# Kernel optimization log

Hardware: AMD Instinct MI355X
Metric: run time of the kernel (lower is better)

Reference implementation:

```python
import jax, jax.numpy as jnp
import numpy as np

B, N, DIM, HEADS = 4, 1024, 1024, 16
DH = DIM // HEADS
SCALE = 1.0 / np.sqrt(DH)
EPS = 1e-6


def clinear(x, Wr, Wi, br, bi):
    # (a+bi)(Wr+Wi i): real = a Wr^T - b Wi^T, imag = a Wi^T + b Wr^T
    xr, xi = x.real, x.imag
    real = xr @ Wr.T - xi @ Wi.T + br
    imag = xr @ Wi.T + xi @ Wr.T + bi
    return jax.lax.complex(real, imag)


def cln(x, gamma, beta):
    # normalize magnitude over last dim, keep phase
    mag = jnp.abs(x)
    phase = jnp.angle(x)
    mean = jnp.mean(mag, axis=-1, keepdims=True)
    var = jnp.var(mag, axis=-1, keepdims=True)
    nm = (mag - mean) / jnp.sqrt(var + EPS)
    nm = nm * gamma + beta
    return jax.lax.complex(nm * jnp.cos(phase), nm * jnp.sin(phase))


def forward(xr, xi, Wq_r, Wq_i, bq_r, bq_i, Wk_r, Wk_i, bk_r, bk_i,
            Wv_r, Wv_i, bv_r, bv_i, Wo_r, Wo_i, bo_r, bo_i,
            gq, beq, gk, bek, gv, bev):
    x = jax.lax.complex(xr, xi)  # [B,N,D] complex64

    def heads(t):
        return t.reshape(B, N, HEADS, DH).transpose(0, 2, 1, 3)  # [B,H,N,dh]

    Q = heads(cln(clinear(x, Wq_r, Wq_i, bq_r, bq_i), gq, beq))
    K = heads(cln(clinear(x, Wk_r, Wk_i, bk_r, bk_i), gk, bek))
    V = heads(cln(clinear(x, Wv_r, Wv_i, bv_r, bv_i), gv, bev))

    Qf = jnp.fft.fft(Q, axis=2, norm='ortho')
    Kf = jnp.fft.fft(K, axis=2, norm='ortho')
    Vf = jnp.fft.fft(V, axis=2, norm='ortho')

    scores = jnp.einsum('bhnd,bhmd->bhnm', Qf, jnp.conj(Kf)) * SCALE
    attn = jax.nn.softmax(scores.real, axis=-1)  # real-valued softmax
    # attn is real; multiply into complex Vf componentwise
    out_f = jax.lax.complex(jnp.einsum('bhnm,bhmd->bhnd', attn, Vf.real),
                            jnp.einsum('bhnm,bhmd->bhnd', attn, Vf.imag))
    out = jnp.fft.ifft(out_f, axis=2, norm='ortho')
    out = out.transpose(0, 2, 1, 3).reshape(B, N, DIM)
    y = clinear(out, Wo_r, Wo_i, bo_r, bo_i)
    # return real||imag concatenated on last axis (float32 view of complex output)
    return jnp.concatenate([y.real, y.imag], axis=-1)


def setup_inputs() -> dict:
    key = jax.random.key(0)
    ks = jax.random.split(key, 16)
    wscale = np.sqrt(2.0 / (DIM + DIM)).astype(np.float32)
    d = {}
    d['xr'] = jax.random.normal(ks[0], (B, N, DIM), jnp.float32)
    d['xi'] = jax.random.normal(ks[1], (B, N, DIM), jnp.float32)
    i = 2
    for name in ('q', 'k', 'v', 'o'):
        d[f'W{name}_r'] = jax.random.normal(ks[i], (DIM, DIM), jnp.float32) * wscale; i += 1
        d[f'W{name}_i'] = jax.random.normal(ks[i], (DIM, DIM), jnp.float32) * wscale; i += 1
        d[f'b{name}_r'] = jnp.zeros((DIM,), jnp.float32)
        d[f'b{name}_i'] = jnp.zeros((DIM,), jnp.float32)
    for name in ('q', 'k', 'v'):
        d[f'g{name}'] = jnp.ones((DIM,), jnp.float32)
        d[f'be{name}'] = jnp.zeros((DIM,), jnp.float32)
    return d


def reference(xr, xi, Wq_r, Wq_i, bq_r, bq_i, Wk_r, Wk_i, bk_r, bk_i,
              Wv_r, Wv_i, bv_r, bv_i, Wo_r, Wo_i, bo_r, bo_i,
              gq, beq, gk, bek, gv, bev):
    return forward(xr, xi, Wq_r, Wq_i, bq_r, bq_i, Wk_r, Wk_i, bk_r, bk_i,
                   Wv_r, Wv_i, bv_r, bv_i, Wo_r, Wo_i, bo_r, bo_i,
                   gq, beq, gk, bek, gv, bev)
```

## Files before the change

### kernel.cpp

```cpp
#include <hip/hip_runtime.h>
#include <math.h>

#define BB 4
#define NN 1024
#define DIMM 1024
#define HHH 16
#define DHH 64
#define BN 4096
#define EPS_LN 1e-6f

typedef __bf16 bf16_t;
typedef __bf16 bf16x8 __attribute__((ext_vector_type(8)));
typedef __bf16 bf16x4 __attribute__((ext_vector_type(4)));
typedef float f32x4 __attribute__((ext_vector_type(4)));
typedef float f32x16 __attribute__((ext_vector_type(16)));
#define MFMA16(a, b, c) __builtin_amdgcn_mfma_f32_16x16x32_bf16(a, b, c, 0, 0, 0)
#define MFMA32(a, b, c) __builtin_amdgcn_mfma_f32_32x32x16_bf16(a, b, c, 0, 0, 0)
#define AS1 __attribute__((address_space(1)))
#define AS3 __attribute__((address_space(3)))

__device__ inline unsigned pk2(float a, float b) {
  union { bf16_t h[2]; unsigned u; } c;
  c.h[0] = (bf16_t)a; c.h[1] = (bf16_t)b;
  return c.u;
}
union U16 { uint4 u; bf16x8 v; };

__global__ __launch_bounds__(256) void pack_x(
    const float* __restrict__ xr, const float* __restrict__ xi,
    bf16_t* __restrict__ out)
{
  int t = blockIdx.x * 256 + threadIdx.x;
  size_t e = (size_t)t * 8;
  int row = (int)(e >> 11), col = (int)(e & 2047);
  const float* src = (col < 1024) ? (xr + (size_t)row * 1024 + col)
                                  : (xi + (size_t)row * 1024 + col - 1024);
  float4 a = *(const float4*)src;
  float4 b = *(const float4*)(src + 4);
  bf16x8 o;
  o[0] = (bf16_t)a.x; o[1] = (bf16_t)a.y; o[2] = (bf16_t)a.z; o[3] = (bf16_t)a.w;
  o[4] = (bf16_t)b.x; o[5] = (bf16_t)b.y; o[6] = (bf16_t)b.z; o[7] = (bf16_t)b.w;
  *(bf16x8*)(out + e) = o;
}

__global__ __launch_bounds__(256) void pack_w4(
    const float* __restrict__ Wqr, const float* __restrict__ Wqi,
    const float* __restrict__ bqr, const float* __restrict__ bqi,
    const float* __restrict__ Wkr, const float* __restrict__ Wki,
    const float* __restrict__ bkr, const float* __restrict__ bki,
    const float* __restrict__ Wvr, const float* __restrict__ Wvi,
    const float* __restrict__ bvr, const float* __restrict__ bvi,
    const float* __restrict__ Wor, const float* __restrict__ Woi,
    const float* __restrict__ bor, const float* __restrict__ boi,
    bf16_t* __restrict__ Wcat4, float* __restrict__ bcat4)
{
  const int p = blockIdx.y;
  const float* Wr; const float* Wi; const float* br; const float* bi;
  if (p == 0)      { Wr = Wqr; Wi = Wqi; br = bqr; bi = bqi; }
  else if (p == 1) { Wr = Wkr; Wi = Wki; br = bkr; bi = bki; }
  else if (p == 2) { Wr = Wvr; Wi = Wvi; br = bvr; bi = bvi; }
  else             { Wr = Wor; Wi = Woi; br = bor; bi = boi; }
  bf16_t* Wcat = Wcat4 + (size_t)p * 2048 * 2048;
  float*  bcat = bcat4 + (size_t)p * 2048;

  int t = blockIdx.x * 256 + threadIdx.x;
  size_t e = (size_t)t * 8;
  int row = (int)(e >> 11), col = (int)(e & 2047);
  const float* src;
  float sgn = 1.f;
  if (row < 1024) {
    if (col < 1024) src = Wr + (size_t)row * 1024 + col;
    else          { src = Wi + (size_t)row * 1024 + col - 1024; sgn = -1.f; }
  } else {
    int r2 = row - 1024;
    if (col < 1024) src = Wi + (size_t)r2 * 1024 + col;
    else            src = Wr + (size_t)r2 * 1024 + col - 1024;
  }
  float4 a = *(const float4*)src;
  float4 b = *(const float4*)(src + 4);
  bf16x8 o;
  o[0] = (bf16_t)(sgn * a.x); o[1] = (bf16_t)(sgn * a.y);
  o[2] = (bf16_t)(sgn * a.z); o[3] = (bf16_t)(sgn * a.w);
  o[4] = (bf16_t)(sgn * b.x); o[5] = (bf16_t)(sgn * b.y);
  o[6] = (bf16_t)(sgn * b.z); o[7] = (bf16_t)(sgn * b.w);
  *(bf16x8*)(Wcat + e) = o;
  if (e < 2048) {
#pragma unroll
    for (int j = 0; j < 8; ++j) {
      int n = (int)e + j;
      bcat[n] = (n < 1024) ? br[n] : bi[n - 1024];
    }
  }
}

__global__ __launch_bounds__(256) void gemm_qkv(
    const bf16_t* __restrict__ A, const bf16_t* __restrict__ Bt,
    const float* __restrict__ bias, bf16_t* __restrict__ C6)
{
  __shared__ bf16_t sA[128 * 64];
  __shared__ bf16_t sB[128 * 64];
  const int tid = threadIdx.x;
  const int w = tid >> 6, l = tid & 63;
  const int lo4 = l & 15, hi = l >> 4;
  const int wr = w >> 1, wc = w & 1;
  const int row0 = blockIdx.y * 128, col0 = blockIdx.x * 128;

  const int srow = (l >> 3);
  const int scol = (l & 7) * 8;
  const bf16_t* gA[4];
  const bf16_t* gB[4];
#pragma unroll
  for (int i = 0; i < 4; ++i) {
    int r = (w * 4 + i) * 8 + srow;
    gA[i] = A  + (size_t)(row0 + r) * 2048 + scol;
    gB[i] = Bt + (size_t)(col0 + r) * 2048 + scol;
  }

  f32x4 acc[4][4] = {};
  for (int k0 = 0; k0 < 2048; k0 += 64) {
    __syncthreads();
#pragma unroll
    for (int i = 0; i < 4; ++i) {
      __builtin_amdgcn_global_load_lds((const AS1 void*)(gA[i] + k0),
                                       (AS3 void*)&sA[(w * 4 + i) * 512], 16, 0, 0);
      __builtin_amdgcn_global_load_lds((const AS1 void*)(gB[i] + k0),
                                       (AS3 void*)&sB[(w * 4 + i) * 512], 16, 0, 0);
    }
    __syncthreads();
#pragma unroll
    for (int kk = 0; kk < 2; ++kk) {
      bf16x8 am[4], bn[4];
#pragma unroll
      for (int i = 0; i < 4; ++i)
        am[i] = *(const bf16x8*)&sA[(wr * 64 + i * 16 + lo4) * 64 + kk * 32 + hi * 8];
#pragma unroll
      for (int j = 0; j < 4; ++j)
        bn[j] = *(const bf16x8*)&sB[(wc * 64 + j * 16 + lo4) * 64 + kk * 32 + hi * 8];
#pragma unroll
      for (int i = 0; i < 4; ++i)
#pragma unroll
        for (int j = 0; j < 4; ++j)
          acc[i][j] = MFMA16(am[i], bn[j], acc[i][j]);
    }
  }
  const int colg0 = col0 + wc * 64;
#pragma unroll
  for (int i = 0; i < 4; ++i) {
#pragma unroll
    for (int j = 0; j < 4; ++j) {
      float bv = bias[colg0 + j * 16 + lo4];
#pragma unroll
      for (int r = 0; r < 4; ++r) {
        int rowg = row0 + wr * 64 + i * 16 + hi * 4 + r;
        C6[(size_t)rowg * 6144 + colg0 + j * 16 + lo4] = (bf16_t)(acc[i][j][r] + bv);
      }
    }
  }
}

__global__ __launch_bounds__(256) void gemm_bf16(
    const bf16_t* __restrict__ A, const bf16_t* __restrict__ Bt,
    const float* __restrict__ bias,
    float* __restrict__ Cr, float* __restrict__ Ci, int ldc)
{
  __shared__ bf16_t sA[128 * 64];
  __shared__ bf16_t sB[128 * 64];
  const int tid = threadIdx.x;
  const int w = tid >> 6, l = tid & 63;
  const int lo4 = l & 15, hi = l >> 4;
  const int wr = w >> 1, wc = w & 1;
  const int row0 = blockIdx.y * 128, col0 = blockIdx.x * 128;

  const int srow = (l >> 3);
  const int scol = (l & 7) * 8;
  const bf16_t* gA[4];
  const bf16_t* gB[4];
#pragma unroll
  for (int i = 0; i < 4; ++i) {
    int r = (w * 4 + i) * 8 + srow;
    gA[i] = A  + (size_t)(row0 + r) * 2048 + scol;
    gB[i] = Bt + (size_t)(col0 + r) * 2048 + scol;
  }

  f32x4 acc[4][4] = {};
  for (int k0 = 0; k0 < 2048; k0 += 64) {
    __syncthreads();
#pragma unroll
    for (int i = 0; i < 4; ++i) {
      __builtin_amdgcn_global_load_lds((const AS1 void*)(gA[i] + k0),
                                       (AS3 void*)&sA[(w * 4 + i) * 512], 16, 0, 0);
      __builtin_amdgcn_global_load_lds((const AS1 void*)(gB[i] + k0),
                                       (AS3 void*)&sB[(w * 4 + i) * 512], 16, 0, 0);
    }
    __syncthreads();
#pragma unroll
    for (int kk = 0; kk < 2; ++kk) {
      bf16x8 am[4], bn[4];
#pragma unroll
      for (int i = 0; i < 4; ++i)
        am[i] = *(const bf16x8*)&sA[(wr * 64 + i * 16 + lo4) * 64 + kk * 32 + hi * 8];
#pragma unroll
      for (int j = 0; j < 4; ++j)
        bn[j] = *(const bf16x8*)&sB[(wc * 64 + j * 16 + lo4) * 64 + kk * 32 + hi * 8];
#pragma unroll
      for (int i = 0; i < 4; ++i)
#pragma unroll
        for (int j = 0; j < 4; ++j)
          acc[i][j] = MFMA16(am[i], bn[j], acc[i][j]);
    }
  }
  const int colg0 = col0 + wc * 64;
  float* Cp = (colg0 < 1024) ? Cr : Ci;
  const int cb = colg0 & 1023;
#pragma unroll
  for (int i = 0; i < 4; ++i) {
#pragma unroll
    for (int j = 0; j < 4; ++j) {
      float bv = bias[colg0 + j * 16 + lo4];
#pragma unroll
      for (int r = 0; r < 4; ++r) {
        int rowg = row0 + wr * 64 + i * 16 + hi * 4 + r;
        Cp[(size_t)rowg * ldc + cb + j * 16 + lo4] = acc[i][j][r] + bv;
      }
    }
  }
}

__global__ __launch_bounds__(256) void ln_stats3(
    const bf16_t* __restrict__ C6, float2* __restrict__ st)
{
  __shared__ float red[8];
  const int row = blockIdx.x;
  const int p = blockIdx.y;
  const int tid = threadIdx.x;
  const bf16_t* pr = C6 + (size_t)row * 6144 + p * 2048;
  const bf16_t* pi = pr + 1024;
  bf16x4 vr = *(const bf16x4*)(pr + tid * 4);
  bf16x4 vi = *(const bf16x4*)(pi + tid * 4);
  float s = 0.f, s2 = 0.f;
#pragma unroll
  for (int t = 0; t < 4; ++t) {
    float a = (float)vr[t], b = (float)vi[t];
    float mg = sqrtf(a * a + b * b);
    s += mg; s2 += mg * mg;
  }
#pragma unroll
  for (int o = 32; o; o >>= 1) { s += __shfl_down(s, o); s2 += __shfl_down(s2, o); }
  if ((tid & 63) == 0) { red[tid >> 6] = s; red[4 + (tid >> 6)] = s2; }
  __syncthreads();
  if (tid == 0) {
    float S = red[0] + red[1] + red[2] + red[3];
    float S2 = red[4] + red[5] + red[6] + red[7];
    float mean = S * (1.f / DIMM);
    float var = S2 * (1.f / DIMM) - mean * mean;
    st[(size_t)p * 4096 + row] = make_float2(mean, rsqrtf(var + EPS_LN));
  }
}

#define LIDX(d_, c_) (((d_) << 10) + ((c_) ^ (((c_) >> 5) & 31) ^ (((d_) & 7) << 2)))

__global__ __launch_bounds__(512) void fft_kernel(
    const bf16_t* __restrict__ inR, const bf16_t* __restrict__ inI,
    bf16_t* __restrict__ outR, bf16_t* __restrict__ outI,
    int in_sb, int in_sh, int in_sn, int in_sd,
    int out_sb, int out_sh, int out_sn,
    float sign, float oscale, int imode, int omode,
    const float2* __restrict__ stats,
    const float* __restrict__ gamma, const float* __restrict__ beta)
{
  __shared__ float lr[8 * 1024], li[8 * 1024];
  __shared__ float2 tw[1024];
  const int tid = threadIdx.x;
  const int dc = blockIdx.x & 7;
  const int bh = blockIdx.x >> 3;
  const int b = bh >> 4, h = bh & 15;
  const bf16_t* bR = inR + (size_t)b * in_sb + (size_t)h * in_sh;
  const bf16_t* bI = inI + (size_t)b * in_sb + (size_t)h * in_sh;
#pragma unroll
  for (int t = tid; t < 1024; t += 512) {
    float ang = sign * 3.14159265358979323846f * (float)t * (1.f / 512.f);
    float sn, cs;
    __sincosf(ang, &sn, &cs);
    tw[t] = make_float2(cs, sn);
  }
  if (imode == 0) {
    float gg[8], bb[8];
    if (stats) {
#pragma unroll
      for (int ds = 0; ds < 8; ++ds) {
        gg[ds] = gamma[h * DHH + dc * 8 + ds];
        bb[ds] = beta[h * DHH + dc * 8 + ds];
      }
    }
#pragma unroll
    for (int rep = 0; rep < 2; ++rep) {
      int n = tid + rep * 512;
      bf16x8 r8 = *(const bf16x8*)(bR + (size_t)n * in_sn + dc * 8);
      bf16x8 i8 = *(const bf16x8*)(bI + (size_t)n * in_sn + dc * 8);
      float ur[8], ui[8];
#pragma unroll
      for (int ds = 0; ds < 8; ++ds) { ur[ds] = (float)r8[ds]; ui[ds] = (float)i8[ds]; }
      if (stats) {
        float2 stv = stats[b * NN + n];
#pragma unroll
        for (int ds = 0; ds < 8; ++ds) {
          float a = ur[ds], c2 = ui[ds];
          float mag = sqrtf(a * a + c2 * c2);
          float nm = (mag - stv.x) * stv.y * gg[ds] + bb[ds];
          if (mag > 0.f) { float sc = nm / mag; ur[ds] = a * sc; ui[ds] = c2 * sc; }
          else           { ur[ds] = nm; ui[ds] = 0.f; }
        }
      }
#pragma unroll
      for (int ds = 0; ds < 8; ++ds) {
        int ax = LIDX(ds, n);
        lr[ax] = ur[ds];
        li[ax] = ui[ds];
      }
    }
  } else {
    const int ds = tid & 7, nb = tid >> 3;
    const bf16_t* pR = bR + (size_t)(dc * 8 + ds) * in_sd + nb * 16;
    const bf16_t* pI = bI + (size_t)(dc * 8 + ds) * in_sd + nb * 16;
    bf16x8 a0 = *(const bf16x8*)pR, a1 = *(const bf16x8*)(pR + 8);
    bf16x8 b0 = *(const bf16x8*)pI, b1 = *(const bf16x8*)(pI + 8);
#pragma unroll
    for (int k = 0; k < 8; ++k) {
      int c = nb * 16 + k;
      lr[LIDX(ds, c)] = (float)a0[k];       li[LIDX(ds, c)] = (float)b0[k];
      lr[LIDX(ds, c + 8)] = (float)a1[k];   li[LIDX(ds, c + 8)] = (float)b1[k];
    }
  }
  __syncthreads();
  const int dsub = tid & 7;
  const int jb = tid >> 3;
  int lq2 = 8;
  for (int st = 0; st < 5; ++st) {
    const int qtr = 1 << lq2;
    const int tmul = 1 << (2 * st);
    for (int jt = 0; jt < 4; ++jt) {
      int j = jb + jt * 64;
      int o = j & (qtr - 1);
      int i0 = ((j >> lq2) << (lq2 + 2)) + o;
      int a0 = LIDX(dsub, i0);
      int a1 = LIDX(dsub, i0 + qtr);
      int a2 = LIDX(dsub, i0 + 2 * qtr);
      int a3 = LIDX(dsub, i0 + 3 * qtr);
      float x0r = lr[a0], x0i = li[a0];
      float x1r = lr[a1], x1i = li[a1];
      float x2r = lr[a2], x2i = li[a2];
      float x3r = lr[a3], x3i = li[a3];
      float ar = x0r + x2r, ai2 = x0i + x2i;
      float br = x0r - x2r, bi  = x0i - x2i;
      float cr = x1r + x3r, ci  = x1i + x3i;
      float dr = x1r - x3r, di  = x1i - x3i;
      float2 t1 = tw[o * tmul];
      float2 t2 = tw[2 * o * tmul];
      float2 t3 = tw[3 * o * tmul];
      lr[a0] = ar + cr;  li[a0] = ai2 + ci;
      float u1r = br - sign * di, u1i = bi + sign * dr;
      lr[a1] = u1r * t1.x - u1i * t1.y;  li[a1] = u1r * t1.y + u1i * t1.x;
      float u2r = ar - cr, u2i = ai2 - ci;
      lr[a2] = u2r * t2.x - u2i * t2.y;  li[a2] = u2r * t2.y + u2i * t2.x;
      float u3r = br + sign * di, u3i = bi - sign * dr;
      lr[a3] = u3r * t3.x - u3i * t3.y;  li[a3] = u3r * t3.y + u3i * t3.x;
    }
    __syncthreads();
    lq2 -= 2;
  }
  bf16_t* oRb = outR + (size_t)b * out_sb + (size_t)h * out_sh;
  bf16_t* oIb = outI + (size_t)b * out_sb + (size_t)h * out_sh;
#pragma unroll
  for (int rep = 0; rep < 2; ++rep) {
    int n = tid + rep * 512;
    int rv2 = __brev((unsigned)n) >> 22;
    int p = ((rv2 & 0x155) << 1) | ((rv2 >> 1) & 0x155);
    float fr[8], fi[8];
#pragma unroll
    for (int ds = 0; ds < 8; ++ds) {
      fr[ds] = lr[LIDX(ds, p)] * oscale;
      fi[ds] = li[LIDX(ds, p)] * oscale;
    }
    if (omode == 1) {
      size_t tb = (size_t)(n >> 5) * 4096;
#pragma unroll
      for (int ds = 0; ds < 8; ++ds) {
        int dch = dc * 8 + ds;
        size_t ga = tb + (size_t)dch * 32 + ((n & 31) ^ (((dch >> 1) & 3) << 3));
        oRb[ga] = (bf16_t)fr[ds];
        oIb[ga] = (bf16_t)fi[ds];
      }
    } else {
      int cb = dc * 8;
      if (omode == 2) cb = (dc ^ (n & 7)) * 8;
      bf16x8 v0, w0;
#pragma unroll
      for (int k = 0; k < 8; ++k) {
        v0[k] = (bf16_t)fr[k];
        w0[k] = (bf16_t)fi[k];
      }
      size_t gb = (size_t)n * out_sn + cb;
      *(bf16x8*)(oRb + gb) = v0;
      *(bf16x8*)(oIb + gb) = w0;
    }
  }
}

__global__ __launch_bounds__(256, 2) void fattn(
    const bf16_t* __restrict__ Qf, const bf16_t* __restrict__ Kfs,
    const bf16_t* __restrict__ Vfs, bf16_t* __restrict__ OT)
{
  __shared__ bf16_t K3[3][4096];
  __shared__ bf16_t V3[3][4096];
  const int tid = threadIdx.x;
  const int w = tid >> 6, l = tid & 63;
  const int lq = l & 31;
  const int h = l >> 5;
  const int i = blockIdx.x;
  const int j = i >> 3;
  const int bh = (i & 7) * 8 + (j >> 3);
  const int q0 = (j & 7) * 128 + w * 32;

  bf16x8 bq[8];
  const bf16_t* qp = Qf + ((size_t)bh * NN + q0 + lq) * 128 + h * 8;
#pragma unroll
  for (int kk = 0; kk < 8; ++kk) bq[kk] = *(const bf16x8*)(qp + kk * 16);

  f32x16 o[4] = {};
  float m = -3e38f, ln = 0.f;

  const bf16_t* kg = Kfs + (size_t)bh * 131072 + w * 1024 + l * 8;
  const bf16_t* vg = Vfs + (size_t)bh * 131072 + w * 1024 + l * 8;
  const int kswz = (lq & 7) << 3;
  const int vswz = ((lq >> 1) & 3) << 3;

#pragma unroll
  for (int tt = 0; tt < 2; ++tt) {
    const bf16_t* kt = kg + (size_t)tt * 4096;
    const bf16_t* vt = vg + (size_t)tt * 4096;
#pragma unroll
    for (int ii = 0; ii < 2; ++ii) {
      __builtin_amdgcn_global_load_lds((const AS1 void*)(kt + ii * 512),
                                       (AS3 void*)&K3[tt][w * 1024 + ii * 512], 16, 0, 0);
      __builtin_amdgcn_global_load_lds((const AS1 void*)(vt + ii * 512),
                                       (AS3 void*)&V3[tt][w * 1024 + ii * 512], 16, 0, 0);
    }
  }
  asm volatile("s_waitcnt vmcnt(4)" ::: "memory");
  __builtin_amdgcn_s_barrier();
  __builtin_amdgcn_sched_barrier(0);

  int cur = 0;
  for (int t = 0; t < 32; ++t) {
    if (t < 30) {
      int nb = cur + 2; if (nb >= 3) nb -= 3;
      const bf16_t* kt = kg + (size_t)(t + 2) * 4096;
      const bf16_t* vt = vg + (size_t)(t + 2) * 4096;
#pragma unroll
      for (int ii = 0; ii < 2; ++ii) {
        __builtin_amdgcn_global_load_lds((const AS1 void*)(kt + ii * 512),
                                         (AS3 void*)&K3[nb][w * 1024 + ii * 512], 16, 0, 0);
        __builtin_amdgcn_global_load_lds((const AS1 void*)(vt + ii * 512),
                                         (AS3 void*)&V3[nb][w * 1024 + ii * 512], 16, 0, 0);
      }
    }

    f32x16 s = {};
#pragma unroll
    for (int kk = 0; kk < 8; ++kk) {
      bf16x8 ak = *(const bf16x8*)&K3[cur][lq * 128 + ((kk * 16 + h * 8) ^ kswz)];
      s = MFMA32(ak, bq[kk], s);
    }

    float pmax = s[0];
#pragma unroll
    for (int r = 1; r < 16; ++r) pmax = fmaxf(pmax, s[r]);
    pmax = fmaxf(pmax, __shfl_xor(pmax, 32));
    if (!__all(pmax - m <= 8.f)) {
      float mnew = fmaxf(m, pmax);
      float alpha = __expf(m - mnew);
      m = mnew;
      ln *= alpha;
#pragma unroll
      for (int db = 0; db < 4; ++db)
#pragma unroll
        for (int r = 0; r < 16; ++r) o[db][r] *= alpha;
    }
    float pf[16];
    float rs = 0.f;
#pragma unroll
    for (int r = 0; r < 16; ++r) { pf[r] = __expf(s[r] - m); rs += pf[r]; }
    rs += __shfl_xor(rs, 32);
    ln += rs;

    unsigned pw[8];
#pragma unroll
    for (int ii = 0; ii < 8; ++ii) pw[ii] = pk2(pf[2 * ii], pf[2 * ii + 1]);
    unsigned r0 = (unsigned)__shfl_xor((int)(h ? pw[0] : pw[2]), 32);
    unsigned r1 = (unsigned)__shfl_xor((int)(h ? pw[1] : pw[3]), 32);
    unsigned r2 = (unsigned)__shfl_xor((int)(h ? pw[4] : pw[6]), 32);
    unsigned r3 = (unsigned)__shfl_xor((int)(h ? pw[5] : pw[7]), 32);
    U16 bp0, bp1;
    bp0.u.x = h ? r0 : pw[0];  bp0.u.y = h ? r1 : pw[1];
    bp0.u.z = h ? pw[2] : r0;  bp0.u.w = h ? pw[3] : r1;
    bp1.u.x = h ? r2 : pw[4];  bp1.u.y = h ? r3 : pw[5];
    bp1.u.z = h ? pw[6] : r2;  bp1.u.w = h ? pw[7] : r3;

#pragma unroll
    for (int db = 0; db < 4; ++db) {
      int r = db * 32 + lq;
      bf16x8 av0 = *(const bf16x8*)&V3[cur][r * 32 + ((h * 8) ^ vswz)];
      bf16x8 av1 = *(const bf16x8*)&V3[cur][r * 32 + ((16 + h * 8) ^ vswz)];
      o[db] = MFMA32(av0, bp0.v, o[db]);
      o[db] = MFMA32(av1, bp1.v, o[db]);
    }

    if (t < 31) {
      if (t < 30) asm volatile("s_waitcnt vmcnt(4)" ::: "memory");
      else        asm volatile("s_waitcnt vmcnt(0)" ::: "memory");
      __builtin_amdgcn_s_barrier();
      __builtin_amdgcn_sched_barrier(0);
    }
    cur = (cur == 2) ? 0 : cur + 1;
  }

  float inv = 1.f / ln;
  const size_t otb = (size_t)bh * 128 * NN + q0 + lq;
#pragma unroll
  for (int db = 0; db < 4; ++db)
#pragma unroll
    for (int r = 0; r < 16; ++r) {
      int dl = (r & 3) + 8 * (r >> 2) + 4 * h;
      OT[otb + (size_t)(db * 32 + dl) * NN] = (bf16_t)(o[db][r] * inv);
    }
}

extern "C" void kernel_launch(void* const* d_in, const int* in_sizes, int n_in,
                              void* d_out, int out_size, void* d_ws, size_t ws_size,
                              hipStream_t stream) {
  const float* xr   = (const float*)d_in[0];
  const float* xi   = (const float*)d_in[1];
  const float* Wqr  = (const float*)d_in[2];
  const float* Wqi  = (const float*)d_in[3];
  const float* bqr  = (const float*)d_in[4];
  const float* bqi  = (const float*)d_in[5];
  const float* Wkr  = (const float*)d_in[6];
  const float* Wki  = (const float*)d_in[7];
  const float* bkr  = (const float*)d_in[8];
  const float* bki  = (const float*)d_in[9];
  const float* Wvr  = (const float*)d_in[10];
  const float* Wvi  = (const float*)d_in[11];
  const float* bvr  = (const float*)d_in[12];
  const float* bvi  = (const float*)d_in[13];
  const float* Wor  = (const float*)d_in[14];
  const float* Woi  = (const float*)d_in[15];
  const float* bor  = (const float*)d_in[16];
  const float* boi  = (const float*)d_in[17];
  const float* gq   = (const float*)d_in[18];
  const float* beq  = (const float*)d_in[19];
  const float* gk   = (const float*)d_in[20];
  const float* bek  = (const float*)d_in[21];
  const float* gv   = (const float*)d_in[22];
  const float* bev  = (const float*)d_in[23];

  char* wp = (char*)d_ws;
  bf16_t* Axaug = (bf16_t*)wp;  wp += (size_t)4096 * 2048 * 2;
  bf16_t* Wcat4 = (bf16_t*)wp;  wp += (size_t)8192 * 2048 * 2;
  float*  bcat4 = (float*)wp;   wp += (size_t)8192 * 4;
  float2* lnst3 = (float2*)wp;  wp += (size_t)3 * 4096 * 8;
  bf16_t* C6    = (bf16_t*)wp;  wp += (size_t)4096 * 6144 * 2;
  bf16_t* Qf    = (bf16_t*)wp;  wp += (size_t)64 * 1024 * 128 * 2;
  bf16_t* Kf    = (bf16_t*)wp;  wp += (size_t)64 * 1024 * 128 * 2;
  bf16_t* VfT   = (bf16_t*)wp;  wp += (size_t)64 * 1024 * 128 * 2;
  bf16_t* OT    = C6;
  bf16_t* Yaug  = Qf;

  const dim3 gQKV(48, 32);
  const dim3 gGemmO(16, 32);
  const int gPackX = (4096 * 2048 / 8) / 256;
  const dim3 gPackW(2048, 4);
  const dim3 gLn(4096, 3);
  const int gFft = 64 * 8;
  const int gAtt = 64 * 8;

  pack_x<<<gPackX, 256, 0, stream>>>(xr, xi, Axaug);
  pack_w4<<<gPackW, 256, 0, stream>>>(Wqr, Wqi, bqr, bqi,
                                      Wkr, Wki, bkr, bki,
                                      Wvr, Wvi, bvr, bvi,
                                      Wor, Woi, bor, boi,
                                      Wcat4, bcat4);

  gemm_qkv<<<gQKV, 256, 0, stream>>>(Axaug, Wcat4, bcat4, C6);
  ln_stats3<<<gLn, 256, 0, stream>>>(C6, lnst3);

  fft_kernel<<<gFft, 512, 0, stream>>>(C6, C6 + 1024, Qf, Qf + 64,
      NN * 6144, DHH, 6144, 1,
      16 * NN * 128, NN * 128, 128,
      -1.0f, 0.03125f * 0.125f, 0, 0, lnst3, gq, beq);
  fft_kernel<<<gFft, 512, 0, stream>>>(C6 + 2048, C6 + 3072, Kf, Kf + 64,
      NN * 6144, DHH, 6144, 1,
      16 * NN * 128, NN * 128, 128,
      -1.0f, 0.03125f, 0, 2, lnst3 + 4096, gk, bek);
  fft_kernel<<<gFft, 512, 0, stream>>>(C6 + 4096, C6 + 5120, VfT, VfT + 2048,
      NN * 6144, DHH, 6144, 1,
      16 * 131072, 131072, 0,
      -1.0f, 0.03125f, 0, 1, lnst3 + 8192, gv, bev);

  fattn<<<gAtt, 256, 0, stream>>>(Qf, Kf, VfT, OT);

  fft_kernel<<<gFft, 512, 0, stream>>>(OT, OT + (size_t)64 * NN, Yaug, Yaug + 1024,
      16 * 128 * NN, 128 * NN, 1, NN,
      NN * 2048, 64, 2048,
      +1.0f, 0.03125f, 1, 0, nullptr, nullptr, nullptr);

  float* yout = (float*)d_out;
  gemm_bf16<<<gGemmO, 256, 0, stream>>>(Yaug,
      Wcat4 + (size_t)3 * 2048 * 2048, bcat4 + 3 * 2048,
      yout, yout + 1024, 2048);
}
```

Measured before the change: 404.3 us.

## Remap GEMM tiles per XCD for L2 reuse and merge Q/K/V FFT launches

```diff
diff --git a/kernel.cpp b/kernel.cpp
--- a/kernel.cpp
+++ b/kernel.cpp
@@ -103,7 +103,12 @@
   const int w = tid >> 6, l = tid & 63;
   const int lo4 = l & 15, hi = l >> 4;
   const int wr = w >> 1, wc = w & 1;
-  const int row0 = blockIdx.y * 128, col0 = blockIdx.x * 128;
+  const int fid = blockIdx.y * 48 + blockIdx.x;
+  const int xcd = fid & 7;
+  const int rr2 = fid >> 3;
+  const int bx = xcd * 6 + (rr2 >> 5);
+  const int by = rr2 & 31;
+  const int row0 = by * 128, col0 = bx * 128;
 
   const int srow = (l >> 3);
   const int scol = (l & 7) * 8;
@@ -169,7 +174,12 @@
   const int w = tid >> 6, l = tid & 63;
   const int lo4 = l & 15, hi = l >> 4;
   const int wr = w >> 1, wc = w & 1;
-  const int row0 = blockIdx.y * 128, col0 = blockIdx.x * 128;
+  const int fid = blockIdx.y * 16 + blockIdx.x;
+  const int xcd = fid & 7;
+  const int rr2 = fid >> 3;
+  const int bx = xcd * 2 + (rr2 >> 5);
+  const int by = rr2 & 31;
+  const int row0 = by * 128, col0 = bx * 128;
 
   const int srow = (l >> 3);
   const int scol = (l & 7) * 8;
@@ -259,14 +269,149 @@
 
 #define LIDX(d_, c_) (((d_) << 10) + ((c_) ^ (((c_) >> 5) & 31) ^ (((d_) & 7) << 2)))
 
+__global__ __launch_bounds__(512) void fft_qkv(
+    const bf16_t* __restrict__ C6,
+    bf16_t* __restrict__ Qf, bf16_t* __restrict__ Kf, bf16_t* __restrict__ VfT,
+    const float2* __restrict__ lnst3,
+    const float* __restrict__ gq, const float* __restrict__ beq,
+    const float* __restrict__ gk, const float* __restrict__ bek,
+    const float* __restrict__ gv, const float* __restrict__ bev)
+{
+  __shared__ float lr[8 * 1024], li[8 * 1024];
+  __shared__ float2 tw[1024];
+  const int tid = threadIdx.x;
+  const int dc = blockIdx.x & 7;
+  const int bh = blockIdx.x >> 3;
+  const int b = bh >> 4, h = bh & 15;
+  const int which = blockIdx.y;
+
+  const bf16_t* inR = C6 + which * 2048;
+  const bf16_t* inI = inR + 1024;
+  const float2* stats = lnst3 + which * 4096;
+  const float* gamma = (which == 0) ? gq : (which == 1) ? gk : gv;
+  const float* beta  = (which == 0) ? beq : (which == 1) ? bek : bev;
+  const float oscale = (which == 0) ? (0.03125f * 0.125f) : 0.03125f;
+  const int omode = (which == 0) ? 0 : (which == 1) ? 2 : 1;
+  bf16_t* outR = (which == 0) ? Qf : (which == 1) ? Kf : VfT;
+  bf16_t* outI = outR + ((which == 2) ? 2048 : 64);
+
+  const bf16_t* bR = inR + (size_t)b * (NN * 6144) + (size_t)h * DHH;
+  const bf16_t* bI = inI + (size_t)b * (NN * 6144) + (size_t)h * DHH;
+#pragma unroll
+  for (int t = tid; t < 1024; t += 512) {
+    float ang = -3.14159265358979323846f * (float)t * (1.f / 512.f);
+    float sn, cs;
+    __sincosf(ang, &sn, &cs);
+    tw[t] = make_float2(cs, sn);
+  }
+  {
+    float gg[8], bb[8];
+#pragma unroll
+    for (int ds = 0; ds < 8; ++ds) {
+      gg[ds] = gamma[h * DHH + dc * 8 + ds];
+      bb[ds] = beta[h * DHH + dc * 8 + ds];
+    }
+#pragma unroll
+    for (int rep = 0; rep < 2; ++rep) {
+      int n = tid + rep * 512;
+      bf16x8 r8 = *(const bf16x8*)(bR + (size_t)n * 6144 + dc * 8);
+      bf16x8 i8 = *(const bf16x8*)(bI + (size_t)n * 6144 + dc * 8);
+      float2 stv = stats[b * NN + n];
+#pragma unroll
+      for (int ds = 0; ds < 8; ++ds) {
+        float a = (float)r8[ds], c2 = (float)i8[ds];
+        float mag = sqrtf(a * a + c2 * c2);
+        float nm = (mag - stv.x) * stv.y * gg[ds] + bb[ds];
+        float re, im;
+        if (mag > 0.f) { float sc = nm / mag; re = a * sc; im = c2 * sc; }
+        else           { re = nm; im = 0.f; }
+        int ax = LIDX(ds, n);
+        lr[ax] = re;
+        li[ax] = im;
+      }
+    }
+  }
+  __syncthreads();
+  const int dsub = tid & 7;
+  const int jb = tid >> 3;
+  int lq2 = 8;
+  for (int st = 0; st < 5; ++st) {
+    const int qtr = 1 << lq2;
+    const int tmul = 1 << (2 * st);
+    for (int jt = 0; jt < 4; ++jt) {
+      int j = jb + jt * 64;
+      int o = j & (qtr - 1);
+      int i0 = ((j >> lq2) << (lq2 + 2)) + o;
+      int a0 = LIDX(dsub, i0);
+      int a1 = LIDX(dsub, i0 + qtr);
+      int a2 = LIDX(dsub, i0 + 2 * qtr);
+      int a3 = LIDX(dsub, i0 + 3 * qtr);
+      float x0r = lr[a0], x0i = li[a0];
+      float x1r = lr[a1], x1i = li[a1];
+      float x2r = lr[a2], x2i = li[a2];
+      float x3r = lr[a3], x3i = li[a3];
+      float ar = x0r + x2r, ai2 = x0i + x2i;
+      float br = x0r - x2r, bi  = x0i - x2i;
+      float cr = x1r + x3r, ci  = x1i + x3i;
+      float dr = x1r - x3r, di  = x1i - x3i;
+      float2 t1 = tw[o * tmul];
+      float2 t2 = tw[2 * o * tmul];
+      float2 t3 = tw[3 * o * tmul];
+      lr[a0] = ar + cr;  li[a0] = ai2 + ci;
+      float u1r = br + di, u1i = bi - dr;
+      lr[a1] = u1r * t1.x - u1i * t1.y;  li[a1] = u1r * t1.y + u1i * t1.x;
+      float u2r = ar - cr, u2i = ai2 - ci;
+      lr[a2] = u2r * t2.x - u2i * t2.y;  li[a2] = u2r * t2.y + u2i * t2.x;
+      float u3r = br - di, u3i = bi + dr;
+      lr[a3] = u3r * t3.x - u3i * t3.y;  li[a3] = u3r * t3.y + u3i * t3.x;
+    }
+    __syncthreads();
+    lq2 -= 2;
+  }
+  bf16_t* oRb = outR + (size_t)b * 2097152 + (size_t)h * 131072;
+  bf16_t* oIb = outI + (size_t)b * 2097152 + (size_t)h * 131072;
+#pragma unroll
+  for (int rep = 0; rep < 2; ++rep) {
+    int n = tid + rep * 512;
+    int rv2 = __brev((unsigned)n) >> 22;
+    int p = ((rv2 & 0x155) << 1) | ((rv2 >> 1) & 0x155);
+    float fr[8], fi[8];
+#pragma unroll
+    for (int ds = 0; ds < 8; ++ds) {
+      fr[ds] = lr[LIDX(ds, p)] * oscale;
+      fi[ds] = li[LIDX(ds, p)] * oscale;
+    }
+    if (omode == 1) {
+      size_t tb = (size_t)(n >> 5) * 4096;
+#pragma unroll
+      for (int ds = 0; ds < 8; ++ds) {
+        int dch = dc * 8 + ds;
+        size_t ga = tb + (size_t)dch * 32 + ((n & 31) ^ (((dch >> 1) & 3) << 3));
+        oRb[ga] = (bf16_t)fr[ds];
+        oIb[ga] = (bf16_t)fi[ds];
+      }
+    } else {
+      int cb = dc * 8;
+      if (omode == 2) cb = (dc ^ (n & 7)) * 8;
+      bf16x8 v0, w0;
+#pragma unroll
+      for (int k = 0; k < 8; ++k) {
+        v0[k] = (bf16_t)fr[k];
+        w0[k] = (bf16_t)fi[k];
+      }
+      size_t gb = (size_t)n * 128 + cb;
+      *(bf16x8*)(oRb + gb) = v0;
+      *(bf16x8*)(oIb + gb) = w0;
+    }
+  }
+}
+
 __global__ __launch_bounds__(512) void fft_kernel(
     const bf16_t* __restrict__ inR, const bf16_t* __restrict__ inI,
     bf16_t* __restrict__ outR, bf16_t* __restrict__ outI,
     int in_sb, int in_sh, int in_sn, int in_sd,
     int out_sb, int out_sh, int out_sn,
-    float sign, float oscale, int imode, int omode,
-    const float2* __restrict__ stats,
-    const float* __restrict__ gamma, const float* __restrict__ beta)
+    float sign, float oscale)
 {
   __shared__ float lr[8 * 1024], li[8 * 1024];
   __shared__ float2 tw[1024];
@@ -283,42 +428,7 @@
     __sincosf(ang, &sn, &cs);
     tw[t] = make_float2(cs, sn);
   }
-  if (imode == 0) {
-    float gg[8], bb[8];
-    if (stats) {
-#pragma unroll
-      for (int ds = 0; ds < 8; ++ds) {
-        gg[ds] = gamma[h * DHH + dc * 8 + ds];
-        bb[ds] = beta[h * DHH + dc * 8 + ds];
-      }
-    }
-#pragma unroll
-    for (int rep = 0; rep < 2; ++rep) {
-      int n = tid + rep * 512;
-      bf16x8 r8 = *(const bf16x8*)(bR + (size_t)n * in_sn + dc * 8);
-      bf16x8 i8 = *(const bf16x8*)(bI + (size_t)n * in_sn + dc * 8);
-      float ur[8], ui[8];
-#pragma unroll
-      for (int ds = 0; ds < 8; ++ds) { ur[ds] = (float)r8[ds]; ui[ds] = (float)i8[ds]; }
-      if (stats) {
-        float2 stv = stats[b * NN + n];
-#pragma unroll
-        for (int ds = 0; ds < 8; ++ds) {
-          float a = ur[ds], c2 = ui[ds];
-          float mag = sqrtf(a * a + c2 * c2);
-          float nm = (mag - stv.x) * stv.y * gg[ds] + bb[ds];
-          if (mag > 0.f) { float sc = nm / mag; ur[ds] = a * sc; ui[ds] = c2 * sc; }
-          else           { ur[ds] = nm; ui[ds] = 0.f; }
-        }
-      }
-#pragma unroll
-      for (int ds = 0; ds < 8; ++ds) {
-        int ax = LIDX(ds, n);
-        lr[ax] = ur[ds];
-        li[ax] = ui[ds];
-      }
-    }
-  } else {
+  {
     const int ds = tid & 7, nb = tid >> 3;
     const bf16_t* pR = bR + (size_t)(dc * 8 + ds) * in_sd + nb * 16;
     const bf16_t* pI = bI + (size_t)(dc * 8 + ds) * in_sd + nb * 16;
@@ -381,28 +491,16 @@
       fr[ds] = lr[LIDX(ds, p)] * oscale;
       fi[ds] = li[LIDX(ds, p)] * oscale;
     }
-    if (omode == 1) {
-      size_t tb = (size_t)(n >> 5) * 4096;
-#pragma unroll
-      for (int ds = 0; ds < 8; ++ds) {
-        int dch = dc * 8 + ds;
-        size_t ga = tb + (size_t)dch * 32 + ((n & 31) ^ (((dch >> 1) & 3) << 3));
-        oRb[ga] = (bf16_t)fr[ds];
-        oIb[ga] = (bf16_t)fi[ds];
-      }
-    } else {
-      int cb = dc * 8;
-      if (omode == 2) cb = (dc ^ (n & 7)) * 8;
-      bf16x8 v0, w0;
-#pragma unroll
-      for (int k = 0; k < 8; ++k) {
-        v0[k] = (bf16_t)fr[k];
-        w0[k] = (bf16_t)fi[k];
-      }
-      size_t gb = (size_t)n * out_sn + cb;
-      *(bf16x8*)(oRb + gb) = v0;
-      *(bf16x8*)(oIb + gb) = w0;
-    }
+    int cb = dc * 8;
+    bf16x8 v0, w0;
+#pragma unroll
+    for (int k = 0; k < 8; ++k) {
+      v0[k] = (bf16_t)fr[k];
+      w0[k] = (bf16_t)fi[k];
+    }
+    size_t gb = (size_t)n * out_sn + cb;
+    *(bf16x8*)(oRb + gb) = v0;
+    *(bf16x8*)(oIb + gb) = w0;
   }
 }
 
@@ -580,6 +678,7 @@
   const int gPackX = (4096 * 2048 / 8) / 256;
   const dim3 gPackW(2048, 4);
   const dim3 gLn(4096, 3);
+  const dim3 gFftQKV(512, 3);
   const int gFft = 64 * 8;
   const int gAtt = 64 * 8;
 
@@ -593,25 +692,15 @@
   gemm_qkv<<<gQKV, 256, 0, stream>>>(Axaug, Wcat4, bcat4, C6);
   ln_stats3<<<gLn, 256, 0, stream>>>(C6, lnst3);
 
-  fft_kernel<<<gFft, 512, 0, stream>>>(C6, C6 + 1024, Qf, Qf + 64,
-      NN * 6144, DHH, 6144, 1,
-      16 * NN * 128, NN * 128, 128,
-      -1.0f, 0.03125f * 0.125f, 0, 0, lnst3, gq, beq);
-  fft_kernel<<<gFft, 512, 0, stream>>>(C6 + 2048, C6 + 3072, Kf, Kf + 64,
-      NN * 6144, DHH, 6144, 1,
-      16 * NN * 128, NN * 128, 128,
-      -1.0f, 0.03125f, 0, 2, lnst3 + 4096, gk, bek);
-  fft_kernel<<<gFft, 512, 0, stream>>>(C6 + 4096, C6 + 5120, VfT, VfT + 2048,
-      NN * 6144, DHH, 6144, 1,
-      16 * 131072, 131072, 0,
-      -1.0f, 0.03125f, 0, 1, lnst3 + 8192, gv, bev);
+  fft_qkv<<<gFftQKV, 512, 0, stream>>>(C6, Qf, Kf, VfT, lnst3,
+                                       gq, beq, gk, bek, gv, bev);
 
   fattn<<<gAtt, 256, 0, stream>>>(Qf, Kf, VfT, OT);
 
   fft_kernel<<<gFft, 512, 0, stream>>>(OT, OT + (size_t)64 * NN, Yaug, Yaug + 1024,
       16 * 128 * NN, 128 * NN, 1, NN,
       NN * 2048, 64, 2048,
-      +1.0f, 0.03125f, 1, 0, nullptr, nullptr, nullptr);
+      +1.0f, 0.03125f);
 
   float* yout = (float*)d_out;
   gemm_bf16<<<gGemmO, 256, 0, stream>>>(Yaug,
```

New measurement: 402.1 us. About the same (-0.5%).
